# Kernel optimization log

Hardware: AMD Instinct MI355X
Metric: run time of the kernel (lower is better)

The kernel has to match this reference:

```python
import jax, jax.numpy as jnp
import numpy as np
import math

L, B, E, H = 1024, 16, 512, 8
NUM_REL = 2 * L - 1  # 2047


def setup_inputs() -> dict:
    key = jax.random.key(0)
    ks = jax.random.split(key, 9)
    s = 0.02
    query = jax.random.normal(ks[0], (L, B, E), dtype=jnp.float32)
    return {
        "query": query,
        "key": jax.random.normal(ks[1], (L, B, E), dtype=jnp.float32),
        "value": jax.random.normal(ks[2], (L, B, E), dtype=jnp.float32),
        "in_proj_weight": jax.random.normal(ks[3], (3 * E, E), dtype=jnp.float32) * s,
        "in_proj_bias": jax.random.normal(ks[4], (3 * E,), dtype=jnp.float32) * s,
        "out_proj_weight": jax.random.normal(ks[5], (E, E), dtype=jnp.float32) * s,
        "out_proj_bias": jax.random.normal(ks[6], (E,), dtype=jnp.float32) * s,
        "rpe_weight_table": jax.random.normal(ks[7], (H, NUM_REL), dtype=jnp.float32) * s,
        "rpe_indices": jax.random.randint(ks[8], (L, L), 0, NUM_REL, dtype=jnp.int32),
    }


def _heads(x, w, b):
    # x: (N, Bn, E), w: (E, E), b: (E,) -> (Bn, H, N, d)
    n, bn, e = x.shape
    d = e // H
    y = jnp.einsum('nbe,fe->nbf', x, w) + b
    return y.reshape(n, bn, H, d).transpose(1, 2, 0, 3)


def reference(query, key, value, in_proj_weight, in_proj_bias, out_proj_weight,
              out_proj_bias, rpe_weight_table, rpe_indices):
    l, bn, e = query.shape
    d = e // H
    wq, wk, wv = jnp.split(in_proj_weight, 3, axis=0)
    bq, bk, bv = jnp.split(in_proj_bias, 3, axis=0)
    q = _heads(query, wq, bq)   # (B, H, L, d)
    k = _heads(key, wk, bk)     # (B, H, S, d)
    v = _heads(value, wv, bv)   # (B, H, S, d)
    q = q / math.sqrt(d)
    # rel-pos bias: gather table -> (H, L, S), broadcast over batch
    bias = rpe_weight_table[:, rpe_indices]
    attn = jnp.einsum('bhld,bhsd->bhls', q, k) + bias[None]
    attn = jax.nn.softmax(attn, axis=-1)
    out = jnp.einsum('bhls,bhsd->bhld', attn, v)   # (B, H, L, d)
    out = out.transpose(2, 0, 1, 3).reshape(l, bn, e)  # (L, B, E)
    out = jnp.einsum('lbe,fe->lbf', out, out_proj_weight) + out_proj_bias
    return out
```

## Files before the change

kernel.cpp:

```cpp
#include <hip/hip_runtime.h>
#include <hip/hip_bf16.h>


#define L_SEQ 1024
#define B_N   16
#define E_DIM 512
#define H_N   8
#define NREL  2047
#define LOG2E 1.44269504f

typedef _Float16 f16;
using half4   = __attribute__((ext_vector_type(4))) _Float16;
using half8   = __attribute__((ext_vector_type(8))) _Float16;
using floatx4 = __attribute__((ext_vector_type(4))) float;

#define LGKM_BARRIER() do {                                   \
    asm volatile("s_waitcnt lgkmcnt(0)" ::: "memory");        \
    __builtin_amdgcn_sched_barrier(0);                        \
    __builtin_amdgcn_s_barrier();                             \
    __builtin_amdgcn_sched_barrier(0);                        \
} while (0)

__device__ __forceinline__ float fast_exp2(float x) {
    return __builtin_amdgcn_exp2f(x);
}

__device__ __forceinline__ half4 cvt4(const float4 a) {
    half4 h;
    h[0] = (f16)a.x; h[1] = (f16)a.y; h[2] = (f16)a.z; h[3] = (f16)a.w;
    return h;
}

__global__ __launch_bounds__(256) void qkv_kernel(
    const float* __restrict__ Xq, const float* __restrict__ Xk, const float* __restrict__ Xv,
    const float* __restrict__ W, const float* __restrict__ Bias,
    f16* __restrict__ Qo, f16* __restrict__ Ko, f16* __restrict__ Vo)
{
    const int flat = blockIdx.x;
    const int xcd  = flat & 7;
    const int slot = flat >> 3;
    const int g    = xcd * 48 + (slot >> 2);
    const int f0   = (slot & 3) << 7;
    const int proj = g >> 7;
    const int n0   = (g & 127) << 7;

    const float* X  = (proj == 0) ? Xq : (proj == 1) ? Xk : Xv;
    const float* Wp = W + (size_t)(proj << 9) * E_DIM;

    __shared__ __align__(16) f16 As[2][128][40];
    __shared__ __align__(16) f16 Bs[2][128][40];

    const int tid  = threadIdx.x;
    const int w    = tid >> 6;
    const int lane = tid & 63;
    const int quad = lane >> 4, c = lane & 15;
    const int wm = (w >> 1) << 6, wn = (w & 1) << 6;

    const int srow = (w << 5) + (lane >> 3);
    const int scol = (lane & 7) << 2;
    const float* Xg = X  + (size_t)(n0 + srow) * E_DIM + scol;
    const float* Wg = Wp + (size_t)(f0 + srow) * E_DIM + scol;

    float4 lx[4], lw[4];
    auto load_tile = [&](int kk) {
#pragma unroll
        for (int i = 0; i < 4; ++i)
            lx[i] = *reinterpret_cast<const float4*>(Xg + (size_t)(i * 8) * E_DIM + kk);
#pragma unroll
        for (int i = 0; i < 4; ++i)
            lw[i] = *reinterpret_cast<const float4*>(Wg + (size_t)(i * 8) * E_DIM + kk);
    };
    auto write_tile = [&](int buf) {
#pragma unroll
        for (int i = 0; i < 4; ++i)
            *reinterpret_cast<half4*>(&As[buf][srow + i * 8][scol]) = cvt4(lx[i]);
#pragma unroll
        for (int i = 0; i < 4; ++i)
            *reinterpret_cast<half4*>(&Bs[buf][srow + i * 8][scol]) = cvt4(lw[i]);
    };

    floatx4 acc[4][4] = {};

    load_tile(0);
    write_tile(0);
    load_tile(32);
    LGKM_BARRIER();

    for (int t = 0; t < 16; ++t) {
        const int cur = t & 1;

        half8 a[4], bfr[4];
#pragma unroll
        for (int mt = 0; mt < 4; ++mt)
            a[mt] = *reinterpret_cast<const half8*>(&As[cur][wm + mt * 16 + c][quad * 8]);
#pragma unroll
        for (int nt = 0; nt < 4; ++nt)
            bfr[nt] = *reinterpret_cast<const half8*>(&Bs[cur][wn + nt * 16 + c][quad * 8]);
#pragma unroll
        for (int mt = 0; mt < 4; ++mt)
#pragma unroll
            for (int nt = 0; nt < 4; ++nt)
                acc[mt][nt] = __builtin_amdgcn_mfma_f32_16x16x32_f16(a[mt], bfr[nt], acc[mt][nt], 0, 0, 0);

        if (t < 15) {
            write_tile(cur ^ 1);
            if (t < 14) load_tile((t + 2) * 32);
        }
        LGKM_BARRIER();
    }

    f16* Dst = (proj == 0) ? Qo : (proj == 1) ? Ko : Vo;
    const float scale = (proj == 0) ? (0.125f * LOG2E) : 1.0f;

#pragma unroll
    for (int nt = 0; nt < 4; ++nt) {
        const int fl = f0 + wn + nt * 16 + c;
        const float bj = Bias[(proj << 9) + fl];
        const int h = fl >> 6, d = fl & 63;
#pragma unroll
        for (int mt = 0; mt < 4; ++mt) {
#pragma unroll
            for (int r = 0; r < 4; ++r) {
                const int n = n0 + wm + mt * 16 + quad * 4 + r;
                const int l = n >> 4, b = n & 15;
                Dst[((((size_t)b * H_N + h) * L_SEQ + l) << 6) + d] =
                    (f16)((acc[mt][nt][r] + bj) * scale);
            }
        }
    }
}

__global__ __launch_bounds__(256) void transpose_v(
    const f16* __restrict__ V, f16* __restrict__ Vt)
{
    const int l0 = blockIdx.x << 6;
    const size_t base = (size_t)blockIdx.y << 16;
    __shared__ __align__(16) f16 T[64][72];
    const int tid = threadIdx.x;
    const int r = tid >> 2, co = (tid & 3) << 4;

    const uint4 a0 = *reinterpret_cast<const uint4*>(V + base + (size_t)(l0 + r) * 64 + co);
    const uint4 a1 = *reinterpret_cast<const uint4*>(V + base + (size_t)(l0 + r) * 64 + co + 8);
    *reinterpret_cast<uint4*>(&T[r][co])     = a0;
    *reinterpret_cast<uint4*>(&T[r][co + 8]) = a1;
    __syncthreads();

    union { f16 h[16]; uint4 u[2]; } pk;
#pragma unroll
    for (int j = 0; j < 16; ++j) pk.h[j] = T[co + j][r];
    *reinterpret_cast<uint4*>(Vt + base + (size_t)r * 1024 + l0 + co)     = pk.u[0];
    *reinterpret_cast<uint4*>(Vt + base + (size_t)r * 1024 + l0 + co + 8) = pk.u[1];
}

__global__ __launch_bounds__(256, 3) void attn_kernel(
    const f16* __restrict__ Q, const f16* __restrict__ K, const f16* __restrict__ Vt,
    const int* __restrict__ RPE, const float* __restrict__ Tab, f16* __restrict__ CTX)
{
    const int flat = blockIdx.x;
    const int xcd  = flat & 7;
    const int slot = flat >> 3;
    const int q0   = (slot & 7) << 7;
    const int bh   = ((slot >> 3) << 3) + xcd;
    const int b = bh >> 3, h = bh & 7;

    const int tid  = threadIdx.x;
    const int w    = tid >> 6;
    const int lane = tid & 63;
    const int quad = lane >> 4, c = lane & 15;

    __shared__ __align__(16) f16 Ks[64][72];
    __shared__ __align__(16) f16 Vts[64][72];
    __shared__ __align__(16) f16 Pw[4][32][72];
    __shared__ float tab[NREL];

    const size_t base = (size_t)bh << 16;

    for (int i = tid; i < NREL; i += 256) tab[i] = Tab[h * NREL + i] * LOG2E;

    const int qg0 = q0 + (w << 5);
    half8 Aq[2][2];
#pragma unroll
    for (int s = 0; s < 2; ++s) {
        const f16* qp = Q + base + (size_t)(qg0 + s * 16 + c) * 64 + quad * 8;
        Aq[s][0] = *reinterpret_cast<const half8*>(qp);
        Aq[s][1] = *reinterpret_cast<const half8*>(qp + 32);
    }

    floatx4 o[2][4] = {};
    float l_part[2][4] = {};

    const int* rp = RPE + (size_t)(qg0 + (quad << 2)) * 1024 + c;

    const int sr = tid >> 2, so = (tid & 3) << 4;
    const f16* kbase = K  + base + (size_t)sr * 64 + so;
    const f16* vbase = Vt + base + (size_t)sr * 1024 + so;

    uint4 pk0 = *reinterpret_cast<const uint4*>(kbase);
    uint4 pk1 = *reinterpret_cast<const uint4*>(kbase + 8);
    uint4 pv0 = *reinterpret_cast<const uint4*>(vbase);
    uint4 pv1 = *reinterpret_cast<const uint4*>(vbase + 8);

    for (int j0 = 0; j0 < L_SEQ; j0 += 64) {
        __syncthreads();
        *reinterpret_cast<uint4*>(&Ks[sr][so])      = pk0;
        *reinterpret_cast<uint4*>(&Ks[sr][so + 8])  = pk1;
        *reinterpret_cast<uint4*>(&Vts[sr][so])     = pv0;
        *reinterpret_cast<uint4*>(&Vts[sr][so + 8]) = pv1;
        __syncthreads();

        if (j0 + 64 < L_SEQ) {
            const f16* kn = kbase + (size_t)(j0 + 64) * 64;
            const f16* vn = vbase + (j0 + 64);
            pk0 = *reinterpret_cast<const uint4*>(kn);
            pk1 = *reinterpret_cast<const uint4*>(kn + 8);
            pv0 = *reinterpret_cast<const uint4*>(vn);
            pv1 = *reinterpret_cast<const uint4*>(vn + 8);
        }

        int idx[2][4][4];
#pragma unroll
        for (int s = 0; s < 2; ++s)
#pragma unroll
            for (int r = 0; r < 4; ++r)
#pragma unroll
                for (int nt = 0; nt < 4; ++nt)
                    idx[s][r][nt] = rp[(size_t)(s * 16 + r) * 1024 + j0 + nt * 16];

        floatx4 sc[2][4];
#pragma unroll
        for (int nt = 0; nt < 4; ++nt) {
            const half8 b0 = *reinterpret_cast<const half8*>(&Ks[nt * 16 + c][quad * 8]);
            const half8 b1 = *reinterpret_cast<const half8*>(&Ks[nt * 16 + c][32 + quad * 8]);
            floatx4 t0 = {}, t1 = {};
            t0 = __builtin_amdgcn_mfma_f32_16x16x32_f16(Aq[0][0], b0, t0, 0, 0, 0);
            t0 = __builtin_amdgcn_mfma_f32_16x16x32_f16(Aq[0][1], b1, t0, 0, 0, 0);
            t1 = __builtin_amdgcn_mfma_f32_16x16x32_f16(Aq[1][0], b0, t1, 0, 0, 0);
            t1 = __builtin_amdgcn_mfma_f32_16x16x32_f16(Aq[1][1], b1, t1, 0, 0, 0);
            sc[0][nt] = t0; sc[1][nt] = t1;
        }

#pragma unroll
        for (int s = 0; s < 2; ++s)
#pragma unroll
            for (int r = 0; r < 4; ++r) {
                float rs = 0.0f;
#pragma unroll
                for (int nt = 0; nt < 4; ++nt) {
                    const float p = fast_exp2(sc[s][nt][r] + tab[idx[s][r][nt]]);
                    rs += p;
                    Pw[w][s * 16 + quad * 4 + r][nt * 16 + c] = (f16)p;
                }
                l_part[s][r] += rs;
            }

        half8 vb[4][2];
#pragma unroll
        for (int nt = 0; nt < 4; ++nt) {
            vb[nt][0] = *reinterpret_cast<const half8*>(&Vts[nt * 16 + c][quad * 8]);
            vb[nt][1] = *reinterpret_cast<const half8*>(&Vts[nt * 16 + c][32 + quad * 8]);
        }
#pragma unroll
        for (int s = 0; s < 2; ++s) {
            const half8 Ap0 = *reinterpret_cast<const half8*>(&Pw[w][s * 16 + c][quad * 8]);
            const half8 Ap1 = *reinterpret_cast<const half8*>(&Pw[w][s * 16 + c][32 + quad * 8]);
#pragma unroll
            for (int nt = 0; nt < 4; ++nt) {
                o[s][nt] = __builtin_amdgcn_mfma_f32_16x16x32_f16(Ap0, vb[nt][0], o[s][nt], 0, 0, 0);
                o[s][nt] = __builtin_amdgcn_mfma_f32_16x16x32_f16(Ap1, vb[nt][1], o[s][nt], 0, 0, 0);
            }
        }
    }

#pragma unroll
    for (int s = 0; s < 2; ++s)
#pragma unroll
        for (int r = 0; r < 4; ++r) {
            float l = l_part[s][r];
            l += __shfl_xor(l, 1); l += __shfl_xor(l, 2);
            l += __shfl_xor(l, 4); l += __shfl_xor(l, 8);
            const float inv = 1.0f / l;
            const int lrow = qg0 + s * 16 + quad * 4 + r;
            f16* dp = CTX + ((size_t)(lrow * 16 + b)) * 512 + h * 64;
#pragma unroll
            for (int nt = 0; nt < 4; ++nt)
                dp[nt * 16 + c] = (f16)(o[s][nt][r] * inv);
        }
}

__global__ __launch_bounds__(256) void out_kernel(
    const f16* __restrict__ X, const float* __restrict__ W, const float* __restrict__ Bias,
    float* __restrict__ Out)
{
    const int flat = blockIdx.x;
    const int xcd  = flat & 7;
    const int slot = flat >> 3;
    const int m    = xcd * 16 + (slot >> 2);
    const int f0   = (slot & 3) << 7;
    const int n0   = m << 7;

    __shared__ __align__(16) f16 As[2][128][40];
    __shared__ __align__(16) f16 Bs[2][128][40];

    const int tid  = threadIdx.x;
    const int w    = tid >> 6;
    const int lane = tid & 63;
    const int quad = lane >> 4, c = lane & 15;
    const int wm = (w >> 1) << 6, wn = (w & 1) << 6;

    const int arow = (w << 5) + (lane >> 2);
    const int acol = (lane & 3) << 3;
    const f16* Xg = X + (size_t)(n0 + arow) * E_DIM + acol;

    const int srow = (w << 5) + (lane >> 3);
    const int scol = (lane & 7) << 2;
    const float* Wg = W + (size_t)(f0 + srow) * E_DIM + scol;

    uint4  la[2];
    float4 lw[4];
    auto load_tile = [&](int kk) {
#pragma unroll
        for (int i = 0; i < 2; ++i)
            la[i] = *reinterpret_cast<const uint4*>(Xg + (size_t)(i * 16) * E_DIM + kk);
#pragma unroll
        for (int i = 0; i < 4; ++i)
            lw[i] = *reinterpret_cast<const float4*>(Wg + (size_t)(i * 8) * E_DIM + kk);
    };
    auto write_tile = [&](int buf) {
#pragma unroll
        for (int i = 0; i < 2; ++i)
            *reinterpret_cast<uint4*>(&As[buf][arow + i * 16][acol]) = la[i];
#pragma unroll
        for (int i = 0; i < 4; ++i)
            *reinterpret_cast<half4*>(&Bs[buf][srow + i * 8][scol]) = cvt4(lw[i]);
    };

    floatx4 acc[4][4] = {};

    load_tile(0);
    write_tile(0);
    load_tile(32);
    LGKM_BARRIER();

    for (int t = 0; t < 16; ++t) {
        const int cur = t & 1;

        half8 a[4], bfr[4];
#pragma unroll
        for (int mt = 0; mt < 4; ++mt)
            a[mt] = *reinterpret_cast<const half8*>(&As[cur][wm + mt * 16 + c][quad * 8]);
#pragma unroll
        for (int nt = 0; nt < 4; ++nt)
            bfr[nt] = *reinterpret_cast<const half8*>(&Bs[cur][wn + nt * 16 + c][quad * 8]);
#pragma unroll
        for (int mt = 0; mt < 4; ++mt)
#pragma unroll
            for (int nt = 0; nt < 4; ++nt)
                acc[mt][nt] = __builtin_amdgcn_mfma_f32_16x16x32_f16(a[mt], bfr[nt], acc[mt][nt], 0, 0, 0);

        if (t < 15) {
            write_tile(cur ^ 1);
            if (t < 14) load_tile((t + 2) * 32);
        }
        LGKM_BARRIER();
    }

#pragma unroll
    for (int nt = 0; nt < 4; ++nt) {
        const int f = f0 + wn + nt * 16 + c;
        const float bj = Bias[f];
#pragma unroll
        for (int mt = 0; mt < 4; ++mt) {
#pragma unroll
            for (int r = 0; r < 4; ++r) {
                const int n = n0 + wm + mt * 16 + quad * 4 + r;
                Out[(size_t)n * E_DIM + f] = acc[mt][nt][r] + bj;
            }
        }
    }
}

extern "C" void kernel_launch(void* const* d_in, const int* in_sizes, int n_in,
                              void* d_out, int out_size, void* d_ws, size_t ws_size,
                              hipStream_t stream) {
    const float* q_in = (const float*)d_in[0];
    const float* k_in = (const float*)d_in[1];
    const float* v_in = (const float*)d_in[2];
    const float* ipw  = (const float*)d_in[3];
    const float* ipb  = (const float*)d_in[4];
    const float* opw  = (const float*)d_in[5];
    const float* opb  = (const float*)d_in[6];
    const float* tab  = (const float*)d_in[7];
    const int*   rpe  = (const int*)d_in[8];
    float* out = (float*)d_out;

    f16* ws   = (f16*)d_ws;
    f16* Q    = ws;
    f16* K    = ws + 8388608;
    f16* Vt   = ws + 16777216;
    f16* Vtmp = ws + 25165824;
    f16* CTX  = ws + 25165824;

    qkv_kernel<<<dim3(1536), 256, 0, stream>>>(q_in, k_in, v_in, ipw, ipb, Q, K, Vtmp);
    transpose_v<<<dim3(16, 128), 256, 0, stream>>>(Vtmp, Vt);
    attn_kernel<<<dim3(1024), 256, 0, stream>>>(Q, K, Vt, rpe, tab, CTX);
    out_kernel<<<dim3(512), 256, 0, stream>>>(CTX, opw, opb, out);
}
```

Baseline: 310.0 us.

## Fuse V transpose into QKV epilogue and double-buffer K/V tiles in attention

The QKV projection kernel now writes V directly in transposed layout by staging the tile through shared memory reused from the GEMM buffers. This removes the separate transpose kernel launch and its extra round trip of V through global memory. The attention kernel double-buffers the K and V^T shared tiles so it needs one barrier per iteration instead of two. To fit the larger LDS footprint, the attention kernel's launch-bounds occupancy hint drops from 3 to 2 blocks.

```diff
diff --git a/kernel.cpp b/kernel.cpp
--- a/kernel.cpp
+++ b/kernel.cpp
@@ -34,7 +34,7 @@
 __global__ __launch_bounds__(256) void qkv_kernel(
     const float* __restrict__ Xq, const float* __restrict__ Xk, const float* __restrict__ Xv,
     const float* __restrict__ W, const float* __restrict__ Bias,
-    f16* __restrict__ Qo, f16* __restrict__ Ko, f16* __restrict__ Vo)
+    f16* __restrict__ Qo, f16* __restrict__ Ko, f16* __restrict__ Vt)
 {
     const int flat = blockIdx.x;
     const int xcd  = flat & 7;
@@ -47,8 +47,10 @@
     const float* X  = (proj == 0) ? Xq : (proj == 1) ? Xk : Xv;
     const float* Wp = W + (size_t)(proj << 9) * E_DIM;
 
-    __shared__ __align__(16) f16 As[2][128][40];
-    __shared__ __align__(16) f16 Bs[2][128][40];
+    __shared__ __align__(16) char smem[40960];
+    auto As = reinterpret_cast<f16(*)[128][40]>(smem);
+    auto Bs = reinterpret_cast<f16(*)[128][40]>(smem + 20480);
+    auto T  = reinterpret_cast<f16(*)[138]>(smem);
 
     const int tid  = threadIdx.x;
     const int w    = tid >> 6;
@@ -109,50 +111,57 @@
         LGKM_BARRIER();
     }
 
-    f16* Dst = (proj == 0) ? Qo : (proj == 1) ? Ko : Vo;
-    const float scale = (proj == 0) ? (0.125f * LOG2E) : 1.0f;
-
-#pragma unroll
-    for (int nt = 0; nt < 4; ++nt) {
-        const int fl = f0 + wn + nt * 16 + c;
-        const float bj = Bias[(proj << 9) + fl];
-        const int h = fl >> 6, d = fl & 63;
-#pragma unroll
-        for (int mt = 0; mt < 4; ++mt) {
-#pragma unroll
-            for (int r = 0; r < 4; ++r) {
-                const int n = n0 + wm + mt * 16 + quad * 4 + r;
-                const int l = n >> 4, b = n & 15;
-                Dst[((((size_t)b * H_N + h) * L_SEQ + l) << 6) + d] =
-                    (f16)((acc[mt][nt][r] + bj) * scale);
+    if (proj != 2) {
+        f16* Dst = (proj == 0) ? Qo : Ko;
+        const float scale = (proj == 0) ? (0.125f * LOG2E) : 1.0f;
+#pragma unroll
+        for (int nt = 0; nt < 4; ++nt) {
+            const int fl = f0 + wn + nt * 16 + c;
+            const float bj = Bias[(proj << 9) + fl];
+            const int h = fl >> 6, d = fl & 63;
+#pragma unroll
+            for (int mt = 0; mt < 4; ++mt) {
+#pragma unroll
+                for (int r = 0; r < 4; ++r) {
+                    const int n = n0 + wm + mt * 16 + quad * 4 + r;
+                    const int l = n >> 4, b = n & 15;
+                    Dst[((((size_t)b * H_N + h) * L_SEQ + l) << 6) + d] =
+                        (f16)((acc[mt][nt][r] + bj) * scale);
+                }
             }
         }
-    }
-}
-
-__global__ __launch_bounds__(256) void transpose_v(
-    const f16* __restrict__ V, f16* __restrict__ Vt)
-{
-    const int l0 = blockIdx.x << 6;
-    const size_t base = (size_t)blockIdx.y << 16;
-    __shared__ __align__(16) f16 T[64][72];
-    const int tid = threadIdx.x;
-    const int r = tid >> 2, co = (tid & 3) << 4;
-
-    const uint4 a0 = *reinterpret_cast<const uint4*>(V + base + (size_t)(l0 + r) * 64 + co);
-    const uint4 a1 = *reinterpret_cast<const uint4*>(V + base + (size_t)(l0 + r) * 64 + co + 8);
-    *reinterpret_cast<uint4*>(&T[r][co])     = a0;
-    *reinterpret_cast<uint4*>(&T[r][co + 8]) = a1;
-    __syncthreads();
-
-    union { f16 h[16]; uint4 u[2]; } pk;
-#pragma unroll
-    for (int j = 0; j < 16; ++j) pk.h[j] = T[co + j][r];
-    *reinterpret_cast<uint4*>(Vt + base + (size_t)r * 1024 + l0 + co)     = pk.u[0];
-    *reinterpret_cast<uint4*>(Vt + base + (size_t)r * 1024 + l0 + co + 8) = pk.u[1];
-}
-
-__global__ __launch_bounds__(256, 3) void attn_kernel(
+    } else {
+#pragma unroll
+        for (int nt = 0; nt < 4; ++nt) {
+            const int fl = wn + nt * 16 + c;
+            const float bj = Bias[(2 << 9) + f0 + fl];
+#pragma unroll
+            for (int mt = 0; mt < 4; ++mt)
+#pragma unroll
+                for (int r = 0; r < 4; ++r)
+                    T[fl][wm + mt * 16 + quad * 4 + r] = (f16)(acc[mt][nt][r] + bj);
+        }
+        __syncthreads();
+
+        const int l0 = n0 >> 4;
+        const int hbase = f0 >> 6;
+#pragma unroll
+        for (int i = 0; i < 8; ++i) {
+            const int idx2 = i * 256 + tid;
+            const int d  = idx2 & 63;
+            const int hh = (idx2 >> 6) & 1;
+            const int bb = idx2 >> 7;
+            const int fl = hh * 64 + d;
+            union { f16 h[8]; uint4 u; } pk;
+#pragma unroll
+            for (int j = 0; j < 8; ++j) pk.h[j] = T[fl][j * 16 + bb];
+            f16* dst = Vt + (((size_t)(bb * H_N + hbase + hh)) << 16) + (size_t)d * 1024 + l0;
+            *reinterpret_cast<uint4*>(dst) = pk.u;
+        }
+    }
+}
+
+__global__ __launch_bounds__(256, 2) void attn_kernel(
     const f16* __restrict__ Q, const f16* __restrict__ K, const f16* __restrict__ Vt,
     const int* __restrict__ RPE, const float* __restrict__ Tab, f16* __restrict__ CTX)
 {
@@ -168,8 +177,8 @@
     const int lane = tid & 63;
     const int quad = lane >> 4, c = lane & 15;
 
-    __shared__ __align__(16) f16 Ks[64][72];
-    __shared__ __align__(16) f16 Vts[64][72];
+    __shared__ __align__(16) f16 Ks[2][64][72];
+    __shared__ __align__(16) f16 Vts[2][64][72];
     __shared__ __align__(16) f16 Pw[4][32][72];
     __shared__ float tab[NREL];
 
@@ -199,22 +208,33 @@
     uint4 pk1 = *reinterpret_cast<const uint4*>(kbase + 8);
     uint4 pv0 = *reinterpret_cast<const uint4*>(vbase);
     uint4 pv1 = *reinterpret_cast<const uint4*>(vbase + 8);
-
-    for (int j0 = 0; j0 < L_SEQ; j0 += 64) {
-        __syncthreads();
-        *reinterpret_cast<uint4*>(&Ks[sr][so])      = pk0;
-        *reinterpret_cast<uint4*>(&Ks[sr][so + 8])  = pk1;
-        *reinterpret_cast<uint4*>(&Vts[sr][so])     = pv0;
-        *reinterpret_cast<uint4*>(&Vts[sr][so + 8]) = pv1;
-        __syncthreads();
-
-        if (j0 + 64 < L_SEQ) {
-            const f16* kn = kbase + (size_t)(j0 + 64) * 64;
-            const f16* vn = vbase + (j0 + 64);
-            pk0 = *reinterpret_cast<const uint4*>(kn);
-            pk1 = *reinterpret_cast<const uint4*>(kn + 8);
-            pv0 = *reinterpret_cast<const uint4*>(vn);
-            pv1 = *reinterpret_cast<const uint4*>(vn + 8);
+    *reinterpret_cast<uint4*>(&Ks[0][sr][so])      = pk0;
+    *reinterpret_cast<uint4*>(&Ks[0][sr][so + 8])  = pk1;
+    *reinterpret_cast<uint4*>(&Vts[0][sr][so])     = pv0;
+    *reinterpret_cast<uint4*>(&Vts[0][sr][so + 8]) = pv1;
+    pk0 = *reinterpret_cast<const uint4*>(kbase + 64 * 64);
+    pk1 = *reinterpret_cast<const uint4*>(kbase + 64 * 64 + 8);
+    pv0 = *reinterpret_cast<const uint4*>(vbase + 64);
+    pv1 = *reinterpret_cast<const uint4*>(vbase + 64 + 8);
+    LGKM_BARRIER();
+
+    for (int t = 0; t < 16; ++t) {
+        const int cur = t & 1;
+        const int j0  = t << 6;
+
+        if (t < 15) {
+            *reinterpret_cast<uint4*>(&Ks[cur ^ 1][sr][so])      = pk0;
+            *reinterpret_cast<uint4*>(&Ks[cur ^ 1][sr][so + 8])  = pk1;
+            *reinterpret_cast<uint4*>(&Vts[cur ^ 1][sr][so])     = pv0;
+            *reinterpret_cast<uint4*>(&Vts[cur ^ 1][sr][so + 8]) = pv1;
+            if (t < 14) {
+                const f16* kn = kbase + (size_t)(t + 2) * 64 * 64;
+                const f16* vn = vbase + (t + 2) * 64;
+                pk0 = *reinterpret_cast<const uint4*>(kn);
+                pk1 = *reinterpret_cast<const uint4*>(kn + 8);
+                pv0 = *reinterpret_cast<const uint4*>(vn);
+                pv1 = *reinterpret_cast<const uint4*>(vn + 8);
+            }
         }
 
         int idx[2][4][4];
@@ -229,8 +249,8 @@
         floatx4 sc[2][4];
 #pragma unroll
         for (int nt = 0; nt < 4; ++nt) {
-            const half8 b0 = *reinterpret_cast<const half8*>(&Ks[nt * 16 + c][quad * 8]);
-            const half8 b1 = *reinterpret_cast<const half8*>(&Ks[nt * 16 + c][32 + quad * 8]);
+            const half8 b0 = *reinterpret_cast<const half8*>(&Ks[cur][nt * 16 + c][quad * 8]);
+            const half8 b1 = *reinterpret_cast<const half8*>(&Ks[cur][nt * 16 + c][32 + quad * 8]);
             floatx4 t0 = {}, t1 = {};
             t0 = __builtin_amdgcn_mfma_f32_16x16x32_f16(Aq[0][0], b0, t0, 0, 0, 0);
             t0 = __builtin_amdgcn_mfma_f32_16x16x32_f16(Aq[0][1], b1, t0, 0, 0, 0);
@@ -256,8 +276,8 @@
         half8 vb[4][2];
 #pragma unroll
         for (int nt = 0; nt < 4; ++nt) {
-            vb[nt][0] = *reinterpret_cast<const half8*>(&Vts[nt * 16 + c][quad * 8]);
-            vb[nt][1] = *reinterpret_cast<const half8*>(&Vts[nt * 16 + c][32 + quad * 8]);
+            vb[nt][0] = *reinterpret_cast<const half8*>(&Vts[cur][nt * 16 + c][quad * 8]);
+            vb[nt][1] = *reinterpret_cast<const half8*>(&Vts[cur][nt * 16 + c][32 + quad * 8]);
         }
 #pragma unroll
         for (int s = 0; s < 2; ++s) {
@@ -269,6 +289,7 @@
                 o[s][nt] = __builtin_amdgcn_mfma_f32_16x16x32_f16(Ap1, vb[nt][1], o[s][nt], 0, 0, 0);
             }
         }
+        LGKM_BARRIER();
     }
 
 #pragma unroll
@@ -397,11 +418,9 @@
     f16* Q    = ws;
     f16* K    = ws + 8388608;
     f16* Vt   = ws + 16777216;
-    f16* Vtmp = ws + 25165824;
     f16* CTX  = ws + 25165824;
 
-    qkv_kernel<<<dim3(1536), 256, 0, stream>>>(q_in, k_in, v_in, ipw, ipb, Q, K, Vtmp);
-    transpose_v<<<dim3(16, 128), 256, 0, stream>>>(Vtmp, Vt);
+    qkv_kernel<<<dim3(1536), 256, 0, stream>>>(q_in, k_in, v_in, ipw, ipb, Q, K, Vt);
     attn_kernel<<<dim3(1024), 256, 0, stream>>>(Q, K, Vt, rpe, tab, CTX);
     out_kernel<<<dim3(512), 256, 0, stream>>>(CTX, opw, opb, out);
 }
```

Measured after the change: 310.8 us. Within noise of the previous version (+0.3%).
